# Performance work log

Measured on AMD Instinct MI355X. Metric: run time of the kernel, lower is better.

Reference implementation:

```python
import jax, jax.numpy as jnp
import numpy as np

D_MODEL = 512
D_FF = 2048
VOCAB = 32000
B, N = 2, 384
EPS = 1e-6


def positional_encoding(n, d):
    pos = np.arange(n)[:, None].astype(np.float64)
    i = np.arange(d)[None, :]
    ang = pos / np.power(10000.0, (2 * (i // 2)) / np.float32(d))
    ang[:, 0::2] = np.sin(ang[:, 0::2])
    ang[:, 1::2] = np.cos(ang[:, 1::2])
    return jnp.asarray(ang, dtype=jnp.float32)  # [n, d]


def layer_norm(x, gamma, beta):
    mu = jnp.mean(x, axis=-1, keepdims=True)
    var = jnp.mean(jnp.square(x - mu), axis=-1, keepdims=True)
    return (x - mu) / jnp.sqrt(var + EPS) * gamma + beta


def setup_inputs() -> dict:
    key = jax.random.key(0)
    ks = jax.random.split(key, 12)
    s = 0.02
    return {
        "tokens": jax.random.randint(ks[0], (B, N), 0, VOCAB, dtype=jnp.int32),
        "emb": jax.random.normal(ks[1], (VOCAB, D_MODEL), jnp.float32) * s,
        "Wq": jax.random.normal(ks[2], (D_MODEL, D_MODEL), jnp.float32) * s,
        "bq": jnp.zeros((D_MODEL,), jnp.float32),
        "Wk": jax.random.normal(ks[3], (D_MODEL, D_MODEL), jnp.float32) * s,
        "bk": jnp.zeros((D_MODEL,), jnp.float32),
        "Wv": jax.random.normal(ks[4], (D_MODEL, D_MODEL), jnp.float32) * s,
        "bv": jnp.zeros((D_MODEL,), jnp.float32),
        "attn_scale": jax.random.normal(ks[5], (D_MODEL,), jnp.float32) * 0.05,
        "Wo": jax.random.normal(ks[6], (D_MODEL, D_MODEL), jnp.float32) * s,
        "bo": jnp.zeros((D_MODEL,), jnp.float32),
        "g1": jnp.ones((D_MODEL,), jnp.float32),
        "beta1": jnp.zeros((D_MODEL,), jnp.float32),
        "W1": jax.random.normal(ks[7], (D_MODEL, D_FF), jnp.float32) * s,
        "bf1": jnp.zeros((D_FF,), jnp.float32),
        "W2": jax.random.normal(ks[8], (D_FF, D_MODEL), jnp.float32) * s,
        "bf2": jnp.zeros((D_MODEL,), jnp.float32),
        "g2": jnp.ones((D_MODEL,), jnp.float32),
        "beta2": jnp.zeros((D_MODEL,), jnp.float32),
    }


def reference(tokens, emb, Wq, bq, Wk, bk, Wv, bv, attn_scale, Wo, bo,
              g1, beta1, W1, bf1, W2, bf2, g2, beta2):
    # Embedding + scaled positional encoding
    x = emb[tokens] * jnp.sqrt(jnp.float32(D_MODEL))  # [B, N, D]
    x = x + positional_encoding(N, D_MODEL)[None, :, :]

    # Additive (Bahdanau) self-attention
    q = x @ Wq + bq
    k = x @ Wk + bk  # note: original swaps key/value Dense layers; math-equivalent
    v = x @ Wv + bv
    # scores[b,i,j] = sum_d scale[d] * tanh(q[b,i,d] + k[b,j,d])  -> [B,N,N]
    scores = jnp.einsum("d,bijd->bij", attn_scale,
                        jnp.tanh(q[:, :, None, :] + k[:, None, :, :]))
    weights = jax.nn.softmax(scores, axis=-1)
    attn = jnp.einsum("bij,bjd->bid", weights, v)
    attn = attn @ Wo + bo
    x = layer_norm(x + attn, g1, beta1)

    # Feedforward + residual + LayerNorm
    h = jax.nn.relu(x @ W1 + bf1)
    y = h @ W2 + bf2
    return layer_norm(x + y, g2, beta2)
```

## Files before the change

kernel.cpp:

```cpp
#include <hip/hip_runtime.h>
#include <hip/hip_bf16.h>
#include <math.h>

#define D_MODEL 512
#define D_FF    2048
#define NBATCH  2
#define NSEQ    384
#define NROWS   (NBATCH * NSEQ)
#define LN_EPS  1e-6f

typedef __attribute__((ext_vector_type(8))) short short8;
typedef __attribute__((ext_vector_type(4))) short short4v;
typedef __attribute__((ext_vector_type(4))) float f32x4;
typedef __hip_bfloat16 bf16;

static __device__ __forceinline__ short bfb(float x) {
    bf16 h = __float2bfloat16(x);
    return *reinterpret_cast<short*>(&h);
}

#define MFMA16(a, b, c) __builtin_amdgcn_mfma_f32_16x16x32_bf16((a), (b), (c), 0, 0, 0)

__global__ __launch_bounds__(256) void prep_kernel(
    const int* __restrict__ tokens, const float* __restrict__ emb,
    const float* __restrict__ Wq, const float* __restrict__ Wk,
    const float* __restrict__ Wv, const float* __restrict__ Wo,
    const float* __restrict__ W1, const float* __restrict__ W2,
    bf16* __restrict__ wqt, bf16* __restrict__ wkt, bf16* __restrict__ wvt,
    bf16* __restrict__ wot, bf16* __restrict__ w1t, bf16* __restrict__ w2t,
    float* __restrict__ x, bf16* __restrict__ xb)
{
    __shared__ float tile[32][33];
    int t = blockIdx.x;

    if (t < 3072) {
        const float* W; bf16* Wt; int K, N, bx, by;
        if (t < 1024) {
            int w = t >> 8, rem = t & 255;
            W  = (w == 0) ? Wq  : (w == 1) ? Wk  : (w == 2) ? Wv  : Wo;
            Wt = (w == 0) ? wqt : (w == 1) ? wkt : (w == 2) ? wvt : wot;
            K = 512; N = 512; bx = rem & 15; by = rem >> 4;
        } else if (t < 2048) {
            int rem = t - 1024;
            W = W1; Wt = w1t; K = 512; N = 2048; bx = rem & 63; by = rem >> 6;
        } else {
            int rem = t - 2048;
            W = W2; Wt = w2t; K = 2048; N = 512; bx = rem & 15; by = rem >> 4;
        }
        int tx = threadIdx.x & 31, ty = threadIdx.x >> 5;
        #pragma unroll
        for (int r = ty; r < 32; r += 8)
            tile[r][tx] = W[(size_t)(by * 32 + r) * N + bx * 32 + tx];
        __syncthreads();
        #pragma unroll
        for (int r = ty; r < 32; r += 8)
            Wt[(size_t)(bx * 32 + r) * K + by * 32 + tx] = __float2bfloat16(tile[tx][r]);
    } else {
        int row = t - 3072;
        int n   = row % NSEQ;
        int tok = tokens[row];
        const float sqrtD = 22.627416997969522f;
        const float ESC   = 0.02595256324130752f;
        for (int d = threadIdx.x; d < D_MODEL; d += 256) {
            float e   = emb[tok * D_MODEL + d] * sqrtD;
            float ang = (float)n * __builtin_amdgcn_exp2f(-(float)(d & ~1) * ESC);
            float pe  = (d & 1) ? __cosf(ang) : __sinf(ang);
            float val = e + pe;
            x [(size_t)row * D_MODEL + d] = val;
            xb[(size_t)row * D_MODEL + d] = __float2bfloat16(val);
        }
    }
}

__global__ __launch_bounds__(256) void qkv_mfma_kernel(
    const bf16* __restrict__ A,
    const bf16* __restrict__ wqt, const bf16* __restrict__ wkt, const bf16* __restrict__ wvt,
    const float* __restrict__ bq, const float* __restrict__ bk, const float* __restrict__ bv,
    float* __restrict__ aexp, float* __restrict__ bexp, bf16* __restrict__ vT)
{
    int z = blockIdx.z;
    const bf16*  Wt   = (z == 0) ? wqt : (z == 1) ? wkt : wvt;
    const float* bias = (z == 0) ? bq  : (z == 1) ? bk  : bv;

    int lane = threadIdx.x & 63, wid = threadIdx.x >> 6;
    int rowBase = blockIdx.y * 32 + (wid >> 1) * 16;
    int colBase = blockIdx.x * 64 + (wid & 1) * 32;

    const bf16* Ap  = A  + (size_t)(rowBase + (lane & 15)) * D_MODEL + ((lane >> 4) << 3);
    const bf16* Bp0 = Wt + (size_t)(colBase + (lane & 15)) * D_MODEL + ((lane >> 4) << 3);
    const bf16* Bp1 = Bp0 + (size_t)16 * D_MODEL;

    f32x4 acc0 = {0.f, 0.f, 0.f, 0.f};
    f32x4 acc1 = {0.f, 0.f, 0.f, 0.f};

    #pragma unroll 4
    for (int k0 = 0; k0 < D_MODEL; k0 += 32) {
        short8 a  = *reinterpret_cast<const short8*>(Ap  + k0);
        short8 b0 = *reinterpret_cast<const short8*>(Bp0 + k0);
        short8 b1 = *reinterpret_cast<const short8*>(Bp1 + k0);
        acc0 = MFMA16(a, b0, acc0);
        acc1 = MFMA16(a, b1, acc1);
    }

    int crow = rowBase + ((lane >> 4) << 2);
    int ccol = colBase + (lane & 15);

    if (z < 2) {
        float* C = (z == 0) ? aexp : bexp;
        #pragma unroll
        for (int r = 0; r < 4; ++r) {
            int row = crow + r;
            #pragma unroll
            for (int j = 0; j < 2; ++j) {
                int col = ccol + j * 16;
                float val = (j == 0 ? acc0[r] : acc1[r]) + bias[col];
                C[(size_t)row * D_MODEL + col] = __expf(2.0f * val);
            }
        }
    } else {
        int bb = crow / NSEQ;
        int jr = crow - bb * NSEQ;
        #pragma unroll
        for (int j = 0; j < 2; ++j) {
            int col = ccol + j * 16;
            short4v pk;
            #pragma unroll
            for (int r = 0; r < 4; ++r)
                pk[r] = bfb((j == 0 ? acc0[r] : acc1[r]) + bias[col]);
            size_t idx = ((size_t)bb * D_MODEL + col) * NSEQ + jr;
            *reinterpret_cast<short4v*>((short*)vT + idx) = pk;
        }
    }
}

__global__ __launch_bounds__(512) void score_kernel(
    const float* __restrict__ aexp, const float* __restrict__ bexp,
    const float* __restrict__ scale, bf16* __restrict__ E,
    float* __restrict__ Sp)
{
    int ig   = blockIdx.x;
    int qt   = blockIdx.y;
    int row0 = ig * 4;
    int b    = row0 / NSEQ;
    int tid  = threadIdx.x;
    int lane = tid & 63, wid = tid >> 6;

    __shared__ float sred[8][4];

    const float* ap = aexp + (size_t)row0 * D_MODEL + lane * 8;
    float a[4][8];
    #pragma unroll
    for (int r = 0; r < 4; ++r) {
        float4 A0 = *(const float4*)(ap + (size_t)r * D_MODEL);
        float4 A1 = *(const float4*)(ap + (size_t)r * D_MODEL + 4);
        a[r][0]=A0.x; a[r][1]=A0.y; a[r][2]=A0.z; a[r][3]=A0.w;
        a[r][4]=A1.x; a[r][5]=A1.y; a[r][6]=A1.z; a[r][7]=A1.w;
    }
    float4 S0 = *(const float4*)(scale + lane * 8);
    float4 S1 = *(const float4*)(scale + lane * 8 + 4);
    float sv[8] = {-2.0f*S0.x,-2.0f*S0.y,-2.0f*S0.z,-2.0f*S0.w,
                   -2.0f*S1.x,-2.0f*S1.y,-2.0f*S1.z,-2.0f*S1.w};

    const float* kb = bexp + (size_t)b * NSEQ * D_MODEL + lane * 8;
    int jb = qt * 96 + wid;

    float es[4] = {0.f, 0.f, 0.f, 0.f};

    #pragma unroll
    for (int half = 0; half < 2; ++half) {
        float uacc[3][4][2];
        #pragma unroll
        for (int t3 = 0; t3 < 3; ++t3)
            #pragma unroll
            for (int r = 0; r < 4; ++r) {
                uacc[t3][r][0] = 0.f; uacc[t3][r][1] = 0.f;
            }

        #pragma unroll
        for (int t3 = 0; t3 < 3; ++t3) {
            int t6 = half * 3 + t3;
            int j0 = jb + t6 * 16;
            int j1 = j0 + 8;
            const float4* kp0 = (const float4*)(kb + (size_t)j0 * D_MODEL);
            const float4* kp1 = (const float4*)(kb + (size_t)j1 * D_MODEL);
            float4 xa = kp0[0], xc = kp0[1];
            float4 ya = kp1[0], yc = kp1[1];
            float b0[8] = {xa.x,xa.y,xa.z,xa.w,xc.x,xc.y,xc.z,xc.w};
            float b1[8] = {ya.x,ya.y,ya.z,ya.w,yc.x,yc.y,yc.z,yc.w};

            #pragma unroll
            for (int up = 0; up < 4; ++up) {
                int d0 = up * 2, d1 = d0 + 1;
                #pragma unroll
                for (int js = 0; js < 2; ++js) {
                    float xx = js ? b1[d0] : b0[d0];
                    float yy = js ? b1[d1] : b0[d1];
                    #pragma unroll
                    for (int r = 0; r < 4; ++r) {
                        float p   = fmaf(a[r][d0], xx, 1.0f);
                        float q   = fmaf(a[r][d1], yy, 1.0f);
                        float num = fmaf(sv[d0], q, sv[d1] * p);
                        uacc[t3][r][js] = fmaf(num, __builtin_amdgcn_rcpf(p * q),
                                               uacc[t3][r][js]);
                    }
                }
            }
        }

        #pragma unroll
        for (int off = 1; off < 64; off <<= 1)
            #pragma unroll
            for (int t3 = 0; t3 < 3; ++t3)
                #pragma unroll
                for (int r = 0; r < 4; ++r) {
                    uacc[t3][r][0] += __shfl_xor(uacc[t3][r][0], off, 64);
                    uacc[t3][r][1] += __shfl_xor(uacc[t3][r][1], off, 64);
                }

        #pragma unroll
        for (int t3 = 0; t3 < 3; ++t3) {
            int t6 = half * 3 + t3;
            int j0 = jb + t6 * 16;
            int j1 = j0 + 8;
            #pragma unroll
            for (int r = 0; r < 4; ++r) {
                float e0 = __expf(uacc[t3][r][0]);
                float e1 = __expf(uacc[t3][r][1]);
                if (lane == 0) {
                    E[(size_t)(row0 + r) * NSEQ + j0] = __float2bfloat16(e0);
                    E[(size_t)(row0 + r) * NSEQ + j1] = __float2bfloat16(e1);
                }
                es[r] += e0 + e1;
            }
        }
    }

    if (lane == 0) {
        sred[wid][0] = es[0]; sred[wid][1] = es[1];
        sred[wid][2] = es[2]; sred[wid][3] = es[3];
    }
    __syncthreads();
    if (tid < 4) {
        float s = 0.0f;
        #pragma unroll
        for (int w = 0; w < 8; ++w) s += sred[w][tid];
        Sp[(size_t)(row0 + tid) * 4 + qt] = s;
    }
}

__global__ __launch_bounds__(256) void pv_mfma_kernel(
    const bf16* __restrict__ E, const bf16* __restrict__ vT,
    const float* __restrict__ Sp, bf16* __restrict__ attnb)
{
    int z = blockIdx.z;
    int lane = threadIdx.x & 63, wid = threadIdx.x >> 6;
    int rowBase = blockIdx.y * 32 + (wid >> 1) * 16;
    int colBase = blockIdx.x * 64 + (wid & 1) * 32;

    const bf16* Ap  = E  + ((size_t)z * NSEQ + rowBase + (lane & 15)) * NSEQ + ((lane >> 4) << 3);
    const bf16* Bp0 = vT + ((size_t)z * D_MODEL + colBase + (lane & 15)) * NSEQ + ((lane >> 4) << 3);
    const bf16* Bp1 = Bp0 + (size_t)16 * NSEQ;

    f32x4 acc0 = {0.f, 0.f, 0.f, 0.f};
    f32x4 acc1 = {0.f, 0.f, 0.f, 0.f};

    #pragma unroll 4
    for (int k0 = 0; k0 < NSEQ; k0 += 32) {
        short8 a  = *reinterpret_cast<const short8*>(Ap  + k0);
        short8 b0 = *reinterpret_cast<const short8*>(Bp0 + k0);
        short8 b1 = *reinterpret_cast<const short8*>(Bp1 + k0);
        acc0 = MFMA16(a, b0, acc0);
        acc1 = MFMA16(a, b1, acc1);
    }

    int crow = rowBase + ((lane >> 4) << 2);
    int ccol = colBase + (lane & 15);
    #pragma unroll
    for (int r = 0; r < 4; ++r) {
        int grow = z * NSEQ + crow + r;
        float4 sp4 = *(const float4*)(Sp + (size_t)grow * 4);
        float Sinv = 1.0f / (sp4.x + sp4.y + sp4.z + sp4.w);
        #pragma unroll
        for (int j = 0; j < 2; ++j)
            attnb[(size_t)grow * D_MODEL + ccol + j * 16] =
                __float2bfloat16((j == 0 ? acc0[r] : acc1[r]) * Sinv);
    }
}

__global__ __launch_bounds__(256) void mfma_gemm_kernel(
    const bf16* __restrict__ A, const bf16* __restrict__ Wt,
    const float* __restrict__ bias, const float* __restrict__ resid,
    float* __restrict__ Cf, bf16* __restrict__ Cb,
    int K, int N, int relu)
{
    int lane = threadIdx.x & 63, wid = threadIdx.x >> 6;
    int rowBase = blockIdx.y * 32 + (wid >> 1) * 16;
    int colBase = blockIdx.x * 64 + (wid & 1) * 32;

    const bf16* Ap  = A  + (size_t)(rowBase + (lane & 15)) * K + ((lane >> 4) << 3);
    const bf16* Bp0 = Wt + (size_t)(colBase + (lane & 15)) * K + ((lane >> 4) << 3);
    const bf16* Bp1 = Bp0 + (size_t)16 * K;

    f32x4 acc0 = {0.f, 0.f, 0.f, 0.f};
    f32x4 acc1 = {0.f, 0.f, 0.f, 0.f};

    #pragma unroll 4
    for (int k0 = 0; k0 < K; k0 += 32) {
        short8 a  = *reinterpret_cast<const short8*>(Ap  + k0);
        short8 b0 = *reinterpret_cast<const short8*>(Bp0 + k0);
        short8 b1 = *reinterpret_cast<const short8*>(Bp1 + k0);
        acc0 = MFMA16(a, b0, acc0);
        acc1 = MFMA16(a, b1, acc1);
    }

    int crow = rowBase + ((lane >> 4) << 2);
    int ccol = colBase + (lane & 15);
    #pragma unroll
    for (int r = 0; r < 4; ++r) {
        int row = crow + r;
        #pragma unroll
        for (int j = 0; j < 2; ++j) {
            int col = ccol + j * 16;
            float val = (j == 0 ? acc0[r] : acc1[r]) + bias[col];
            if (resid) val += resid[(size_t)row * N + col];
            if (relu)  val = fmaxf(val, 0.0f);
            if (Cf) Cf[(size_t)row * N + col] = val;
            if (Cb) Cb[(size_t)row * N + col] = __float2bfloat16(val);
        }
    }
}

__global__ __launch_bounds__(256) void ffdown_kernel(
    const bf16* __restrict__ A, const bf16* __restrict__ Wt,
    const float* __restrict__ bias, const float* __restrict__ resid,
    float* __restrict__ y0, float* __restrict__ y1)
{
    int z = blockIdx.z;
    int kbeg = z * (D_FF / 2);
    int lane = threadIdx.x & 63, wid = threadIdx.x >> 6;
    int rowBase = blockIdx.y * 32 + (wid >> 1) * 16;
    int colBase = blockIdx.x * 64 + (wid & 1) * 32;

    const bf16* Ap  = A  + (size_t)(rowBase + (lane & 15)) * D_FF + kbeg + ((lane >> 4) << 3);
    const bf16* Bp0 = Wt + (size_t)(colBase + (lane & 15)) * D_FF + kbeg + ((lane >> 4) << 3);
    const bf16* Bp1 = Bp0 + (size_t)16 * D_FF;

    f32x4 acc0 = {0.f, 0.f, 0.f, 0.f};
    f32x4 acc1 = {0.f, 0.f, 0.f, 0.f};

    #pragma unroll 4
    for (int k0 = 0; k0 < D_FF / 2; k0 += 32) {
        short8 a  = *reinterpret_cast<const short8*>(Ap  + k0);
        short8 b0 = *reinterpret_cast<const short8*>(Bp0 + k0);
        short8 b1 = *reinterpret_cast<const short8*>(Bp1 + k0);
        acc0 = MFMA16(a, b0, acc0);
        acc1 = MFMA16(a, b1, acc1);
    }

    int crow = rowBase + ((lane >> 4) << 2);
    int ccol = colBase + (lane & 15);
    #pragma unroll
    for (int r = 0; r < 4; ++r) {
        int row = crow + r;
        #pragma unroll
        for (int j = 0; j < 2; ++j) {
            int col = ccol + j * 16;
            float val = (j == 0 ? acc0[r] : acc1[r]);
            if (z == 0) {
                val += bias[col] + resid[(size_t)row * D_MODEL + col];
                y0[(size_t)row * D_MODEL + col] = val;
            } else {
                y1[(size_t)row * D_MODEL + col] = val;
            }
        }
    }
}

__global__ __launch_bounds__(256) void ln_kernel(
    const float* __restrict__ in, const float* __restrict__ in2,
    const float* __restrict__ gamma, const float* __restrict__ beta,
    float* __restrict__ out, bf16* __restrict__ outb)
{
    int row = blockIdx.x;
    int tid = threadIdx.x;
    int lane = tid & 63, wid = tid >> 6;
    __shared__ float red[4];

    float v0 = in[(size_t)row * D_MODEL + tid];
    float v1 = in[(size_t)row * D_MODEL + tid + 256];
    if (in2) {
        v0 += in2[(size_t)row * D_MODEL + tid];
        v1 += in2[(size_t)row * D_MODEL + tid + 256];
    }

    float s = v0 + v1;
    #pragma unroll
    for (int off = 32; off; off >>= 1) s += __shfl_xor(s, off, 64);
    if (lane == 0) red[wid] = s;
    __syncthreads();
    if (tid == 0) red[0] = red[0] + red[1] + red[2] + red[3];
    __syncthreads();
    float mu = red[0] * (1.0f / D_MODEL);
    __syncthreads();

    float d0 = v0 - mu, d1 = v1 - mu;
    float s2 = d0 * d0 + d1 * d1;
    #pragma unroll
    for (int off = 32; off; off >>= 1) s2 += __shfl_xor(s2, off, 64);
    if (lane == 0) red[wid] = s2;
    __syncthreads();
    if (tid == 0) red[0] = red[0] + red[1] + red[2] + red[3];
    __syncthreads();
    float var = red[0] * (1.0f / D_MODEL);
    float inv = rsqrtf(var + LN_EPS);

    float o0 = d0 * inv * gamma[tid] + beta[tid];
    float o1 = d1 * inv * gamma[tid + 256] + beta[tid + 256];
    out[(size_t)row * D_MODEL + tid]       = o0;
    out[(size_t)row * D_MODEL + tid + 256] = o1;
    if (outb) {
        outb[(size_t)row * D_MODEL + tid]       = __float2bfloat16(o0);
        outb[(size_t)row * D_MODEL + tid + 256] = __float2bfloat16(o1);
    }
}

extern "C" void kernel_launch(void* const* d_in, const int* in_sizes, int n_in,
                              void* d_out, int out_size, void* d_ws, size_t ws_size,
                              hipStream_t stream)
{
    const int*   tokens = (const int*)  d_in[0];
    const float* emb    = (const float*)d_in[1];
    const float* Wq     = (const float*)d_in[2];
    const float* bq     = (const float*)d_in[3];
    const float* Wk     = (const float*)d_in[4];
    const float* bk     = (const float*)d_in[5];
    const float* Wv     = (const float*)d_in[6];
    const float* bv     = (const float*)d_in[7];
    const float* ascale = (const float*)d_in[8];
    const float* Wo     = (const float*)d_in[9];
    const float* bo     = (const float*)d_in[10];
    const float* g1     = (const float*)d_in[11];
    const float* beta1  = (const float*)d_in[12];
    const float* W1     = (const float*)d_in[13];
    const float* bf1    = (const float*)d_in[14];
    const float* W2     = (const float*)d_in[15];
    const float* bf2    = (const float*)d_in[16];
    const float* g2     = (const float*)d_in[17];
    const float* beta2  = (const float*)d_in[18];

    float* out = (float*)d_out;
    float* ws  = (float*)d_ws;

    const size_t SZ = (size_t)NROWS * D_MODEL;

    float* x0   = ws;
    float* aexp = ws + 1 * SZ;
    float* bexp = ws + 2 * SZ;
    float* t1 = aexp;
    float* x1 = bexp;
    float* y0 = x1;
    float* y1 = x0;

    bf16* x0b   = (bf16*)(ws + 3 * SZ);
    bf16* attnb = x0b + SZ;
    bf16* x1b   = attnb + SZ;
    bf16* hb    = x1b + SZ;
    bf16* Eb    = hb + (size_t)NROWS * D_FF;
    bf16* vTb   = Eb + (size_t)NBATCH * NSEQ * NSEQ;
    bf16* wqt   = vTb + (size_t)NBATCH * D_MODEL * NSEQ;
    bf16* wkt   = wqt + (size_t)D_MODEL * D_MODEL;
    bf16* wvt   = wkt + (size_t)D_MODEL * D_MODEL;
    bf16* wot   = wvt + (size_t)D_MODEL * D_MODEL;
    bf16* w1t   = wot + (size_t)D_MODEL * D_MODEL;
    bf16* w2t   = w1t + (size_t)D_MODEL * D_FF;
    float* Sp   = (float*)(w2t + (size_t)D_FF * D_MODEL);

    prep_kernel<<<3072 + NROWS, 256, 0, stream>>>(
        tokens, emb, Wq, Wk, Wv, Wo, W1, W2,
        wqt, wkt, wvt, wot, w1t, w2t, x0, x0b);

    qkv_mfma_kernel<<<dim3(D_MODEL / 64, NROWS / 32, 3), 256, 0, stream>>>(
        x0b, wqt, wkt, wvt, bq, bk, bv, aexp, bexp, vTb);

    score_kernel<<<dim3(NROWS / 4, 4), 512, 0, stream>>>(aexp, bexp, ascale, Eb, Sp);

    pv_mfma_kernel<<<dim3(D_MODEL / 64, NSEQ / 32, NBATCH), 256, 0, stream>>>(
        Eb, vTb, Sp, attnb);

    mfma_gemm_kernel<<<dim3(D_MODEL / 64, NROWS / 32), 256, 0, stream>>>(
        attnb, wot, bo, x0, t1, nullptr, D_MODEL, D_MODEL, 0);

    ln_kernel<<<NROWS, 256, 0, stream>>>(t1, nullptr, g1, beta1, x1, x1b);

    mfma_gemm_kernel<<<dim3(D_FF / 64, NROWS / 32), 256, 0, stream>>>(
        x1b, w1t, bf1, nullptr, nullptr, hb, D_MODEL, D_FF, 1);

    ffdown_kernel<<<dim3(D_MODEL / 64, NROWS / 32, 2), 256, 0, stream>>>(
        hb, w2t, bf2, x1, y0, y1);

    ln_kernel<<<NROWS, 256, 0, stream>>>(y0, y1, g2, beta2, out, nullptr);
}
```

Before: 123.8 us.

## Transpose key-exp layout and map score lanes to key positions, removing wave reductions

The key projection output is now written in a blocked-transposed layout ([b][d/8][j][8]), so each lane of the score kernel owns one key position j and loops over the full model dimension serially. This removes the per-tile 64-lane shuffle reductions over d and the shared-memory reduction. The score grid changes to 8 rows per block across 3 j-chunk blocks, and the partial-sum layout grows to 6 chunks per row. In exchange, each thread does 512-long serial accumulation, holds fewer query rows in registers, and reads the query and scale vectors as wave-uniform broadcast loads.

```diff
diff --git a/kernel.cpp b/kernel.cpp
--- a/kernel.cpp
+++ b/kernel.cpp
@@ -76,7 +76,7 @@
     const bf16* __restrict__ A,
     const bf16* __restrict__ wqt, const bf16* __restrict__ wkt, const bf16* __restrict__ wvt,
     const float* __restrict__ bq, const float* __restrict__ bk, const float* __restrict__ bv,
-    float* __restrict__ aexp, float* __restrict__ bexp, bf16* __restrict__ vT)
+    float* __restrict__ aexp, float* __restrict__ bexpT, bf16* __restrict__ vT)
 {
     int z = blockIdx.z;
     const bf16*  Wt   = (z == 0) ? wqt : (z == 1) ? wkt : wvt;
@@ -105,8 +105,7 @@
     int crow = rowBase + ((lane >> 4) << 2);
     int ccol = colBase + (lane & 15);
 
-    if (z < 2) {
-        float* C = (z == 0) ? aexp : bexp;
+    if (z == 0) {
         #pragma unroll
         for (int r = 0; r < 4; ++r) {
             int row = crow + r;
@@ -114,7 +113,21 @@
             for (int j = 0; j < 2; ++j) {
                 int col = ccol + j * 16;
                 float val = (j == 0 ? acc0[r] : acc1[r]) + bias[col];
-                C[(size_t)row * D_MODEL + col] = __expf(2.0f * val);
+                aexp[(size_t)row * D_MODEL + col] = __expf(2.0f * val);
+            }
+        }
+    } else if (z == 1) {
+        int bb = crow / NSEQ;
+        int jr = crow - bb * NSEQ;
+        #pragma unroll
+        for (int j = 0; j < 2; ++j) {
+            int col = ccol + j * 16;
+            size_t base = (((size_t)bb * (D_MODEL / 8) + (col >> 3)) * NSEQ + jr) * 8
+                        + (col & 7);
+            #pragma unroll
+            for (int r = 0; r < 4; ++r) {
+                float val = (j == 0 ? acc0[r] : acc1[r]) + bias[col];
+                bexpT[base + (size_t)r * 8] = __expf(2.0f * val);
             }
         }
     } else {
@@ -134,117 +147,75 @@
 }
 
 __global__ __launch_bounds__(512) void score_kernel(
-    const float* __restrict__ aexp, const float* __restrict__ bexp,
+    const float* __restrict__ aexp, const float* __restrict__ bexpT,
     const float* __restrict__ scale, bf16* __restrict__ E,
     float* __restrict__ Sp)
 {
-    int ig   = blockIdx.x;
-    int qt   = blockIdx.y;
-    int row0 = ig * 4;
+    int w    = threadIdx.x >> 6, lane = threadIdx.x & 63;
+    int row0 = blockIdx.x * 8 + (w >> 1) * 2;
+    int chunkj = blockIdx.y * 2 + (w & 1);
+    int j    = chunkj * 64 + lane;
     int b    = row0 / NSEQ;
-    int tid  = threadIdx.x;
-    int lane = tid & 63, wid = tid >> 6;
-
-    __shared__ float sred[8][4];
-
-    const float* ap = aexp + (size_t)row0 * D_MODEL + lane * 8;
-    float a[4][8];
-    #pragma unroll
-    for (int r = 0; r < 4; ++r) {
-        float4 A0 = *(const float4*)(ap + (size_t)r * D_MODEL);
-        float4 A1 = *(const float4*)(ap + (size_t)r * D_MODEL + 4);
-        a[r][0]=A0.x; a[r][1]=A0.y; a[r][2]=A0.z; a[r][3]=A0.w;
-        a[r][4]=A1.x; a[r][5]=A1.y; a[r][6]=A1.z; a[r][7]=A1.w;
-    }
-    float4 S0 = *(const float4*)(scale + lane * 8);
-    float4 S1 = *(const float4*)(scale + lane * 8 + 4);
-    float sv[8] = {-2.0f*S0.x,-2.0f*S0.y,-2.0f*S0.z,-2.0f*S0.w,
-                   -2.0f*S1.x,-2.0f*S1.y,-2.0f*S1.z,-2.0f*S1.w};
-
-    const float* kb = bexp + (size_t)b * NSEQ * D_MODEL + lane * 8;
-    int jb = qt * 96 + wid;
-
-    float es[4] = {0.f, 0.f, 0.f, 0.f};
-
-    #pragma unroll
-    for (int half = 0; half < 2; ++half) {
-        float uacc[3][4][2];
-        #pragma unroll
-        for (int t3 = 0; t3 < 3; ++t3)
-            #pragma unroll
-            for (int r = 0; r < 4; ++r) {
-                uacc[t3][r][0] = 0.f; uacc[t3][r][1] = 0.f;
+
+    const float* a0 = aexp + (size_t)row0 * D_MODEL;
+    const float* a1 = a0 + D_MODEL;
+    const float* bT = bexpT + ((size_t)b * (D_MODEL / 8) * NSEQ + j) * 8;
+
+    float u0a = 0.f, u0b = 0.f, u1a = 0.f, u1b = 0.f;
+
+    #pragma unroll 2
+    for (int c = 0; c < D_MODEL / 8; ++c) {
+        int d0 = c * 8;
+        const float* bp = bT + (size_t)c * NSEQ * 8;
+        float4 bA = *(const float4*)(bp);
+        float4 bB = *(const float4*)(bp + 4);
+        float4 aA0 = *(const float4*)(a0 + d0);
+        float4 aB0 = *(const float4*)(a0 + d0 + 4);
+        float4 aA1 = *(const float4*)(a1 + d0);
+        float4 aB1 = *(const float4*)(a1 + d0 + 4);
+        float4 sA  = *(const float4*)(scale + d0);
+        float4 sB  = *(const float4*)(scale + d0 + 4);
+
+        float bb[8]  = {bA.x,bA.y,bA.z,bA.w,bB.x,bB.y,bB.z,bB.w};
+        float aa0[8] = {aA0.x,aA0.y,aA0.z,aA0.w,aB0.x,aB0.y,aB0.z,aB0.w};
+        float aa1[8] = {aA1.x,aA1.y,aA1.z,aA1.w,aB1.x,aB1.y,aB1.z,aB1.w};
+        float sv[8]  = {sA.x,sA.y,sA.z,sA.w,sB.x,sB.y,sB.z,sB.w};
+
+        #pragma unroll
+        for (int up = 0; up < 4; ++up) {
+            int e0 = up * 2, e1 = e0 + 1;
+            {
+                float p   = fmaf(aa0[e0], bb[e0], 1.0f);
+                float q   = fmaf(aa0[e1], bb[e1], 1.0f);
+                float num = fmaf(sv[e0], q, sv[e1] * p);
+                if (up & 1) u0b = fmaf(num, __builtin_amdgcn_rcpf(p * q), u0b);
+                else        u0a = fmaf(num, __builtin_amdgcn_rcpf(p * q), u0a);
             }
-
-        #pragma unroll
-        for (int t3 = 0; t3 < 3; ++t3) {
-            int t6 = half * 3 + t3;
-            int j0 = jb + t6 * 16;
-            int j1 = j0 + 8;
-            const float4* kp0 = (const float4*)(kb + (size_t)j0 * D_MODEL);
-            const float4* kp1 = (const float4*)(kb + (size_t)j1 * D_MODEL);
-            float4 xa = kp0[0], xc = kp0[1];
-            float4 ya = kp1[0], yc = kp1[1];
-            float b0[8] = {xa.x,xa.y,xa.z,xa.w,xc.x,xc.y,xc.z,xc.w};
-            float b1[8] = {ya.x,ya.y,ya.z,ya.w,yc.x,yc.y,yc.z,yc.w};
-
-            #pragma unroll
-            for (int up = 0; up < 4; ++up) {
-                int d0 = up * 2, d1 = d0 + 1;
-                #pragma unroll
-                for (int js = 0; js < 2; ++js) {
-                    float xx = js ? b1[d0] : b0[d0];
-                    float yy = js ? b1[d1] : b0[d1];
-                    #pragma unroll
-                    for (int r = 0; r < 4; ++r) {
-                        float p   = fmaf(a[r][d0], xx, 1.0f);
-                        float q   = fmaf(a[r][d1], yy, 1.0f);
-                        float num = fmaf(sv[d0], q, sv[d1] * p);
-                        uacc[t3][r][js] = fmaf(num, __builtin_amdgcn_rcpf(p * q),
-                                               uacc[t3][r][js]);
-                    }
-                }
+            {
+                float p   = fmaf(aa1[e0], bb[e0], 1.0f);
+                float q   = fmaf(aa1[e1], bb[e1], 1.0f);
+                float num = fmaf(sv[e0], q, sv[e1] * p);
+                if (up & 1) u1b = fmaf(num, __builtin_amdgcn_rcpf(p * q), u1b);
+                else        u1a = fmaf(num, __builtin_amdgcn_rcpf(p * q), u1a);
             }
         }
-
-        #pragma unroll
-        for (int off = 1; off < 64; off <<= 1)
-            #pragma unroll
-            for (int t3 = 0; t3 < 3; ++t3)
-                #pragma unroll
-                for (int r = 0; r < 4; ++r) {
-                    uacc[t3][r][0] += __shfl_xor(uacc[t3][r][0], off, 64);
-                    uacc[t3][r][1] += __shfl_xor(uacc[t3][r][1], off, 64);
-                }
-
-        #pragma unroll
-        for (int t3 = 0; t3 < 3; ++t3) {
-            int t6 = half * 3 + t3;
-            int j0 = jb + t6 * 16;
-            int j1 = j0 + 8;
-            #pragma unroll
-            for (int r = 0; r < 4; ++r) {
-                float e0 = __expf(uacc[t3][r][0]);
-                float e1 = __expf(uacc[t3][r][1]);
-                if (lane == 0) {
-                    E[(size_t)(row0 + r) * NSEQ + j0] = __float2bfloat16(e0);
-                    E[(size_t)(row0 + r) * NSEQ + j1] = __float2bfloat16(e1);
-                }
-                es[r] += e0 + e1;
-            }
-        }
-    }
-
+    }
+
+    float e0 = __expf(-2.0f * (u0a + u0b));
+    float e1 = __expf(-2.0f * (u1a + u1b));
+
+    E[(size_t)row0 * NSEQ + j]       = __float2bfloat16(e0);
+    E[(size_t)(row0 + 1) * NSEQ + j] = __float2bfloat16(e1);
+
+    float s0 = e0, s1 = e1;
+    #pragma unroll
+    for (int off = 1; off < 64; off <<= 1) {
+        s0 += __shfl_xor(s0, off, 64);
+        s1 += __shfl_xor(s1, off, 64);
+    }
     if (lane == 0) {
-        sred[wid][0] = es[0]; sred[wid][1] = es[1];
-        sred[wid][2] = es[2]; sred[wid][3] = es[3];
-    }
-    __syncthreads();
-    if (tid < 4) {
-        float s = 0.0f;
-        #pragma unroll
-        for (int w = 0; w < 8; ++w) s += sred[w][tid];
-        Sp[(size_t)(row0 + tid) * 4 + qt] = s;
+        Sp[(size_t)row0 * 8 + chunkj]       = s0;
+        Sp[(size_t)(row0 + 1) * 8 + chunkj] = s1;
     }
 }
 
@@ -278,8 +249,10 @@
     #pragma unroll
     for (int r = 0; r < 4; ++r) {
         int grow = z * NSEQ + crow + r;
-        float4 sp4 = *(const float4*)(Sp + (size_t)grow * 4);
-        float Sinv = 1.0f / (sp4.x + sp4.y + sp4.z + sp4.w);
+        float4 sp4 = *(const float4*)(Sp + (size_t)grow * 8);
+        float s5 = Sp[(size_t)grow * 8 + 4];
+        float s6 = Sp[(size_t)grow * 8 + 5];
+        float Sinv = 1.0f / (sp4.x + sp4.y + sp4.z + sp4.w + s5 + s6);
         #pragma unroll
         for (int j = 0; j < 2; ++j)
             attnb[(size_t)grow * D_MODEL + ccol + j * 16] =
@@ -453,11 +426,11 @@
 
     const size_t SZ = (size_t)NROWS * D_MODEL;
 
-    float* x0   = ws;
-    float* aexp = ws + 1 * SZ;
-    float* bexp = ws + 2 * SZ;
+    float* x0    = ws;
+    float* aexp  = ws + 1 * SZ;
+    float* bexpT = ws + 2 * SZ;
     float* t1 = aexp;
-    float* x1 = bexp;
+    float* x1 = bexpT;
     float* y0 = x1;
     float* y1 = x0;
 
@@ -480,9 +453,9 @@
         wqt, wkt, wvt, wot, w1t, w2t, x0, x0b);
 
     qkv_mfma_kernel<<<dim3(D_MODEL / 64, NROWS / 32, 3), 256, 0, stream>>>(
-        x0b, wqt, wkt, wvt, bq, bk, bv, aexp, bexp, vTb);
-
-    score_kernel<<<dim3(NROWS / 4, 4), 512, 0, stream>>>(aexp, bexp, ascale, Eb, Sp);
+        x0b, wqt, wkt, wvt, bq, bk, bv, aexp, bexpT, vTb);
+
+    score_kernel<<<dim3(NROWS / 8, 3), 512, 0, stream>>>(aexp, bexpT, ascale, Eb, Sp);
 
     pv_mfma_kernel<<<dim3(D_MODEL / 64, NSEQ / 32, NBATCH), 256, 0, stream>>>(
         Eb, vTb, Sp, attnb);
```

Measured after the change: 141.9 us. 1.15x slower.

## Fuse first LayerNorm into FF-up GEMM with LDS-staged normalized rows

Applied to the files above, without the earlier changes.

Removes the standalone LayerNorm kernel after the output projection and folds it into the FF-up GEMM: each block normalizes its 32 rows of t1 into shared memory as bf16 and then runs the MFMA loop with A read from LDS. Only blocks in the first column write the fp32 x1 residual used later. This saves one launch and the x1b bf16 round trip, at the cost of every one of the 32 column blocks recomputing the LayerNorm for the same rows and a larger LDS footprint per block.

```diff
diff --git a/kernel.cpp b/kernel.cpp
--- a/kernel.cpp
+++ b/kernel.cpp
@@ -290,8 +290,7 @@
 __global__ __launch_bounds__(256) void mfma_gemm_kernel(
     const bf16* __restrict__ A, const bf16* __restrict__ Wt,
     const float* __restrict__ bias, const float* __restrict__ resid,
-    float* __restrict__ Cf, bf16* __restrict__ Cb,
-    int K, int N, int relu)
+    float* __restrict__ Cf, int K, int N)
 {
     int lane = threadIdx.x & 63, wid = threadIdx.x >> 6;
     int rowBase = blockIdx.y * 32 + (wid >> 1) * 16;
@@ -321,11 +320,101 @@
         #pragma unroll
         for (int j = 0; j < 2; ++j) {
             int col = ccol + j * 16;
-            float val = (j == 0 ? acc0[r] : acc1[r]) + bias[col];
-            if (resid) val += resid[(size_t)row * N + col];
-            if (relu)  val = fmaxf(val, 0.0f);
-            if (Cf) Cf[(size_t)row * N + col] = val;
-            if (Cb) Cb[(size_t)row * N + col] = __float2bfloat16(val);
+            float val = (j == 0 ? acc0[r] : acc1[r]) + bias[col]
+                      + resid[(size_t)row * N + col];
+            Cf[(size_t)row * N + col] = val;
+        }
+    }
+}
+
+__global__ __launch_bounds__(256) void ffup_ln_kernel(
+    const float* __restrict__ t1, const float* __restrict__ g1,
+    const float* __restrict__ beta1, const bf16* __restrict__ w1t,
+    const float* __restrict__ bf1, float* __restrict__ x1,
+    bf16* __restrict__ hb)
+{
+    int rowBase = blockIdx.y * 32;
+    int colBase = blockIdx.x * 64;
+    int tid  = threadIdx.x;
+    int lane = tid & 63, wid = tid >> 6;
+
+    __shared__ bf16 x1S[32][D_MODEL + 8];
+
+    float4 G0 = *(const float4*)(g1 + lane * 8);
+    float4 G1 = *(const float4*)(g1 + lane * 8 + 4);
+    float4 B0 = *(const float4*)(beta1 + lane * 8);
+    float4 B1 = *(const float4*)(beta1 + lane * 8 + 4);
+    float gv[8] = {G0.x,G0.y,G0.z,G0.w,G1.x,G1.y,G1.z,G1.w};
+    float bv[8] = {B0.x,B0.y,B0.z,B0.w,B1.x,B1.y,B1.z,B1.w};
+
+    #pragma unroll
+    for (int rr = 0; rr < 8; ++rr) {
+        int lrow = wid * 8 + rr;
+        size_t grow = (size_t)(rowBase + lrow);
+        const float* rp = t1 + grow * D_MODEL + lane * 8;
+        float4 V0 = *(const float4*)rp;
+        float4 V1 = *(const float4*)(rp + 4);
+        float v[8] = {V0.x,V0.y,V0.z,V0.w,V1.x,V1.y,V1.z,V1.w};
+
+        float s = ((v[0]+v[1])+(v[2]+v[3])) + ((v[4]+v[5])+(v[6]+v[7]));
+        #pragma unroll
+        for (int off = 1; off < 64; off <<= 1) s += __shfl_xor(s, off, 64);
+        float mu = s * (1.0f / D_MODEL);
+
+        float s2 = 0.0f;
+        #pragma unroll
+        for (int u = 0; u < 8; ++u) { float d = v[u] - mu; s2 += d * d; }
+        #pragma unroll
+        for (int off = 1; off < 64; off <<= 1) s2 += __shfl_xor(s2, off, 64);
+        float inv = rsqrtf(s2 * (1.0f / D_MODEL) + LN_EPS);
+
+        short4v pk0, pk1;
+        float o[8];
+        #pragma unroll
+        for (int u = 0; u < 8; ++u) {
+            o[u] = (v[u] - mu) * inv * gv[u] + bv[u];
+            if (u < 4) pk0[u] = bfb(o[u]); else pk1[u - 4] = bfb(o[u]);
+        }
+        *reinterpret_cast<short4v*>(&x1S[lrow][lane * 8])     = pk0;
+        *reinterpret_cast<short4v*>(&x1S[lrow][lane * 8 + 4]) = pk1;
+        if (blockIdx.x == 0) {
+            float4 w0 = {o[0], o[1], o[2], o[3]};
+            float4 w1 = {o[4], o[5], o[6], o[7]};
+            *(float4*)(x1 + grow * D_MODEL + lane * 8)     = w0;
+            *(float4*)(x1 + grow * D_MODEL + lane * 8 + 4) = w1;
+        }
+    }
+    __syncthreads();
+
+    int wrow = (wid >> 1) * 16;
+    int wcol = colBase + (wid & 1) * 32;
+    int arow = lane & 15, koff = (lane >> 4) << 3;
+
+    const bf16* Bp0 = w1t + (size_t)(wcol + arow) * D_MODEL + koff;
+    const bf16* Bp1 = Bp0 + (size_t)16 * D_MODEL;
+
+    f32x4 acc0 = {0.f, 0.f, 0.f, 0.f};
+    f32x4 acc1 = {0.f, 0.f, 0.f, 0.f};
+
+    #pragma unroll 4
+    for (int k0 = 0; k0 < D_MODEL; k0 += 32) {
+        short8 a  = *reinterpret_cast<const short8*>(&x1S[wrow + arow][k0 + koff]);
+        short8 b0 = *reinterpret_cast<const short8*>(Bp0 + k0);
+        short8 b1 = *reinterpret_cast<const short8*>(Bp1 + k0);
+        acc0 = MFMA16(a, b0, acc0);
+        acc1 = MFMA16(a, b1, acc1);
+    }
+
+    int crow = rowBase + wrow + ((lane >> 4) << 2);
+    int ccol = wcol + (lane & 15);
+    #pragma unroll
+    for (int r = 0; r < 4; ++r) {
+        int row = crow + r;
+        #pragma unroll
+        for (int j = 0; j < 2; ++j) {
+            int col = ccol + j * 16;
+            float val = fmaxf((j == 0 ? acc0[r] : acc1[r]) + bf1[col], 0.0f);
+            hb[(size_t)row * D_FF + col] = __float2bfloat16(val);
         }
     }
 }
@@ -379,7 +468,7 @@
 __global__ __launch_bounds__(256) void ln_kernel(
     const float* __restrict__ in, const float* __restrict__ in2,
     const float* __restrict__ gamma, const float* __restrict__ beta,
-    float* __restrict__ out, bf16* __restrict__ outb)
+    float* __restrict__ out)
 {
     int row = blockIdx.x;
     int tid = threadIdx.x;
@@ -414,14 +503,8 @@
     float var = red[0] * (1.0f / D_MODEL);
     float inv = rsqrtf(var + LN_EPS);
 
-    float o0 = d0 * inv * gamma[tid] + beta[tid];
-    float o1 = d1 * inv * gamma[tid + 256] + beta[tid + 256];
-    out[(size_t)row * D_MODEL + tid]       = o0;
-    out[(size_t)row * D_MODEL + tid + 256] = o1;
-    if (outb) {
-        outb[(size_t)row * D_MODEL + tid]       = __float2bfloat16(o0);
-        outb[(size_t)row * D_MODEL + tid + 256] = __float2bfloat16(o1);
-    }
+    out[(size_t)row * D_MODEL + tid]       = d0 * inv * gamma[tid] + beta[tid];
+    out[(size_t)row * D_MODEL + tid + 256] = d1 * inv * gamma[tid + 256] + beta[tid + 256];
 }
 
 extern "C" void kernel_launch(void* const* d_in, const int* in_sizes, int n_in,
@@ -463,8 +546,7 @@
 
     bf16* x0b   = (bf16*)(ws + 3 * SZ);
     bf16* attnb = x0b + SZ;
-    bf16* x1b   = attnb + SZ;
-    bf16* hb    = x1b + SZ;
+    bf16* hb    = attnb + SZ;
     bf16* Eb    = hb + (size_t)NROWS * D_FF;
     bf16* vTb   = Eb + (size_t)NBATCH * NSEQ * NSEQ;
     bf16* wqt   = vTb + (size_t)NBATCH * D_MODEL * NSEQ;
@@ -488,15 +570,13 @@
         Eb, vTb, Sp, attnb);
 
     mfma_gemm_kernel<<<dim3(D_MODEL / 64, NROWS / 32), 256, 0, stream>>>(
-        attnb, wot, bo, x0, t1, nullptr, D_MODEL, D_MODEL, 0);
-
-    ln_kernel<<<NROWS, 256, 0, stream>>>(t1, nullptr, g1, beta1, x1, x1b);
-
-    mfma_gemm_kernel<<<dim3(D_FF / 64, NROWS / 32), 256, 0, stream>>>(
-        x1b, w1t, bf1, nullptr, nullptr, hb, D_MODEL, D_FF, 1);
+        attnb, wot, bo, x0, t1, D_MODEL, D_MODEL);
+
+    ffup_ln_kernel<<<dim3(D_FF / 64, NROWS / 32), 256, 0, stream>>>(
+        t1, g1, beta1, w1t, bf1, x1, hb);
 
     ffdown_kernel<<<dim3(D_MODEL / 64, NROWS / 32, 2), 256, 0, stream>>>(
         hb, w2t, bf2, x1, y0, y1);
 
-    ln_kernel<<<NROWS, 256, 0, stream>>>(y0, y1, g2, beta2, out, nullptr);
-}
+    ln_kernel<<<NROWS, 256, 0, stream>>>(y0, y1, g2, beta2, out);
+}
```

Result: faster. 119.7 us (-3.4%).
